# Kernel tuning notes

Measured on AMD Instinct MI355X. Metric: run time of the kernel, lower is better.

Reference implementation:

```python
import jax, jax.numpy as jnp
import numpy as np

EMBED = 256      # input_size
DOWN = 64        # expert hidden_size
NUM_EXPERTS = 10
TOPK = 2
GATE_SCALE = 0.5
LOSS_COEF = 1.0
CV_EPS = 1e-10


def setup_inputs() -> dict:
    key = jax.random.key(0)
    ks = jax.random.split(key, 6)
    B, N = 16, 4096
    x = jax.random.normal(ks[0], (B, N, EMBED), jnp.float32)
    # gating weight (Parameter in torch; random here so top-k is non-degenerate)
    w_gate = jax.random.normal(ks[1], (EMBED, NUM_EXPERTS), jnp.float32) * 0.02
    # expert MLP params: fc1 (EMBED->DOWN), relu, fc2 (DOWN->EMBED)
    w1 = jax.random.normal(ks[2], (NUM_EXPERTS, EMBED, DOWN), jnp.float32) * (1.0 / np.sqrt(EMBED))
    b1 = jnp.zeros((NUM_EXPERTS, DOWN), jnp.float32)
    w2 = jax.random.normal(ks[3], (NUM_EXPERTS, DOWN, EMBED), jnp.float32) * (1.0 / np.sqrt(DOWN))
    b2 = jnp.zeros((NUM_EXPERTS, EMBED), jnp.float32)
    return {"x": x, "w_gate": w_gate, "w1": w1, "b1": b1, "w2": w2, "b2": b2}


def _cv_squared(v):
    # torch: x.var() / (x.mean()**2 + eps), unbiased variance
    return jnp.var(v, ddof=1) / (jnp.mean(v) ** 2 + CV_EPS)


def reference(x, w_gate, w1, b1, w2, b2):
    B, N, D = x.shape
    xt = x.reshape(B * N, D)                      # (T, D)
    T = B * N

    # --- noisy top-k gating (eval mode: no noise) ---
    logits = xt @ w_gate                          # (T, E)
    top_logits, top_idx = jax.lax.top_k(logits, TOPK)
    top_gates = jax.nn.softmax(top_logits, axis=-1)
    gates = jnp.zeros((T, NUM_EXPERTS), x.dtype).at[
        jnp.arange(T)[:, None], top_idx].set(top_gates)   # (T, E), sparse rows

    importance = gates.sum(axis=0)                               # (E,)
    load = jnp.sum(gates > 0, axis=0).astype(x.dtype)            # (E,)
    aux_loss = (_cv_squared(importance) + _cv_squared(load)) * LOSS_COEF

    # --- expert FFN dispatch+combine (dense equivalent: zero gates kill terms) ---
    h = jax.nn.relu(jnp.einsum('td,edh->teh', xt, w1) + b1[None])   # (T, E, DOWN)
    ye = jnp.einsum('teh,eho->teo', h, w2) + b2[None]               # (T, E, D)
    y = jnp.einsum('te,teo->to', gates, ye)                         # (T, D)

    out = y.reshape(B, N, -1)
    # self-KD L1 loss vs zeros, computed BEFORE gate_scale is applied
    kd_loss = jnp.mean(jnp.abs(out))
    moe_loss = aux_loss + kd_loss
    return out * GATE_SCALE, moe_loss
```

## Files before the change

kernel.cpp:

```cpp
#include <hip/hip_runtime.h>
#include <hip/hip_bf16.h>

#define T_TOKENS 65536
#define EMBED 256
#define DOWN 64
#define NE 10
#define NPAIR 100
#define MAXQ 1280
#define XROW 72

typedef __attribute__((ext_vector_type(8))) short short8;
typedef __attribute__((ext_vector_type(4))) float f32x4;

__device__ inline unsigned short f2bf(float f) {
    unsigned u = __builtin_bit_cast(unsigned, f);
    u += 0x7fff + ((u >> 16) & 1);
    return (unsigned short)(u >> 16);
}
__device__ inline float bf2f(unsigned short h) {
    unsigned u = ((unsigned)h) << 16;
    return __builtin_bit_cast(float, u);
}

__global__ __launch_bounds__(256) void pack_kernel(
    const float* __restrict__ w1, const float* __restrict__ w2,
    unsigned short* __restrict__ w1ph, unsigned short* __restrict__ w1pl,
    unsigned short* __restrict__ w2ph, unsigned short* __restrict__ w2pl)
{
    int gid = blockIdx.x * 256 + threadIdx.x;
    int lane = gid & 63;
    int fid = gid >> 6;
    int n16 = lane & 15;
    int kbase = ((lane >> 4) & 3) * 8;
    if (fid < 320) {
        int kb = fid & 7, ect = fid >> 3;
        int ct = ect & 3, e = ect >> 2;
        int n = ct * 16 + n16;
        int k0 = kb * 32 + kbase;
#pragma unroll
        for (int j = 0; j < 8; ++j) {
            float v = w1[((size_t)e * EMBED + k0 + j) * DOWN + n];
            unsigned short h = f2bf(v);
            w1ph[(size_t)fid * 512 + lane * 8 + j] = h;
            w1pl[(size_t)fid * 512 + lane * 8 + j] = f2bf(v - bf2f(h));
        }
    } else if (fid < 640) {
        int f2 = fid - 320;
        int kb = f2 & 1, ect = f2 >> 1;
        int ct = ect & 15, e = ect >> 4;
        int n = ct * 16 + n16;
        int k0 = kb * 32 + kbase;
#pragma unroll
        for (int j = 0; j < 8; ++j) {
            float v = w2[((size_t)e * DOWN + k0 + j) * EMBED + n];
            unsigned short h = f2bf(v);
            w2ph[(size_t)f2 * 512 + lane * 8 + j] = h;
            w2pl[(size_t)f2 * 512 + lane * 8 + j] = f2bf(v - bf2f(h));
        }
    }
}

__global__ __launch_bounds__(256) void gating_kernel(
    const float* __restrict__ x, const float* __restrict__ wg,
    int* __restrict__ pcount, float* __restrict__ importance,
    int* __restrict__ btok, float* __restrict__ bg0)
{
    __shared__ float Xs[2][256 * 33];
    __shared__ int lcount[NPAIR];
    __shared__ int gbase[NPAIR];
    __shared__ float limp[16];
    int tid = threadIdx.x;
    if (tid < NPAIR) lcount[tid] = 0;
    if (tid < 16) limp[tid] = 0.f;

    int tokbase = blockIdx.x * 256;
    const float4* x4 = (const float4*)x;
    int rbase = tid >> 3, c4 = tid & 7;

    float4 pre[8];
#pragma unroll
    for (int i = 0; i < 8; ++i)
        pre[i] = x4[(size_t)(tokbase + i * 32 + rbase) * 64 + c4];

    float acc[NE];
#pragma unroll
    for (int e = 0; e < NE; e++) acc[e] = 0.f;

    for (int cc = 0; cc < 8; ++cc) {
        float* buf = Xs[cc & 1];
#pragma unroll
        for (int i = 0; i < 8; ++i) {
            float* d = &buf[(i * 32 + rbase) * 33 + c4 * 4];
            d[0] = pre[i].x; d[1] = pre[i].y; d[2] = pre[i].z; d[3] = pre[i].w;
        }
        if (cc < 7) {
#pragma unroll
            for (int i = 0; i < 8; ++i)
                pre[i] = x4[(size_t)(tokbase + i * 32 + rbase) * 64 + (cc + 1) * 8 + c4];
        }
        __syncthreads();
        const float* wgc = wg + cc * 32 * NE;
#pragma unroll
        for (int c = 0; c < 32; ++c) {
            float xv = buf[tid * 33 + c];
#pragma unroll
            for (int e = 0; e < NE; ++e)
                acc[e] = fmaf(xv, wgc[c * NE + e], acc[e]);
        }
    }

    float l0 = -INFINITY, l1 = -INFINITY;
    int i0 = 0, i1 = 0;
#pragma unroll
    for (int e = 0; e < NE; e++) {
        float v = acc[e];
        if (v > l0) { l1 = l0; i1 = i0; l0 = v; i0 = e; }
        else if (v > l1) { l1 = v; i1 = e; }
    }
    float ex = __expf(l1 - l0);
    float g0 = 1.f / (1.f + ex);

    int p = i0 * NE + i1;
    int lp = atomicAdd(&lcount[p], 1);
    atomicAdd(&limp[i0], g0);
    atomicAdd(&limp[i1], 1.f - g0);
    __syncthreads();
    if (tid < NPAIR) {
        int c = lcount[tid];
        gbase[tid] = c ? atomicAdd(&pcount[tid], c) : 0;
    }
    if (tid < NE) atomicAdd(&importance[tid], limp[tid]);
    __syncthreads();
    int pos = gbase[p] + lp;
    btok[p * T_TOKENS + pos] = tokbase + tid;
    bg0[p * T_TOKENS + pos] = g0;
}

__global__ void queue_kernel(const int* __restrict__ pcount,
                             int* __restrict__ qp, int* __restrict__ qs, int* __restrict__ nq)
{
    if (threadIdx.x == 0) {
        int n = 0;
        for (int p = 0; p < NPAIR; p++) {
            int c = pcount[p];
            for (int s = 0; s < c; s += 64) { qp[n] = p; qs[n] = s; n++; }
        }
        *nq = n;
    }
}

__global__ __launch_bounds__(256, 3) void expert_kernel(
    const float* __restrict__ x,
    const unsigned short* __restrict__ w1ph, const unsigned short* __restrict__ w1pl,
    const unsigned short* __restrict__ w2ph, const unsigned short* __restrict__ w2pl,
    const float* __restrict__ b1, const float* __restrict__ b2,
    const int* __restrict__ pcount, const int* __restrict__ qp, const int* __restrict__ qs,
    const int* __restrict__ nq,
    const int* __restrict__ btok, const float* __restrict__ bg0,
    float* __restrict__ out, float* __restrict__ kdpart)
{
    int bid = blockIdx.x;
    if (bid >= *nq) return;
    int p = qp[bid], s = qs[bid];
    int e0 = p / NE, e1 = p - e0 * NE;
    int m = min(64, pcount[p] - s);

    __shared__ __align__(16) unsigned short Xh[64 * XROW], Xl[64 * XROW];
    __shared__ __align__(16) unsigned short H0h[4096], H0l[4096];
    __shared__ __align__(16) unsigned short H1h[4096], H1l[4096];
    __shared__ int toks[64];
    __shared__ float gv0s[64], gv1s[64];
    __shared__ float kdw[4];

    int tid = threadIdx.x;
    if (tid < 64) {
        int v = 0; float g = 0.f;
        if (tid < m) {
            v = btok[p * T_TOKENS + s + tid];
            g = bg0[p * T_TOKENS + s + tid];
        }
        toks[tid] = v;
        gv0s[tid] = g;
        gv1s[tid] = (tid < m) ? (1.f - g) : 0.f;
    }
    __syncthreads();

    int lane = tid & 63, wv = tid >> 6;
    int ln15 = lane & 15, quad = lane >> 4;
    int srow = tid >> 2, sc0 = (tid & 3) * 16;
    const float* xrow = x + (size_t)toks[srow] * EMBED;
    bool srow_ok = srow < m;

    f32x4 a10[4], a11[4];
#pragma unroll
    for (int rt = 0; rt < 4; ++rt) { a10[rt] = (f32x4){0,0,0,0}; a11[rt] = (f32x4){0,0,0,0}; }

    const unsigned short* w1h0 = w1ph + (((size_t)e0 * 4 + wv) * 8) * 512;
    const unsigned short* w1l0 = w1pl + (((size_t)e0 * 4 + wv) * 8) * 512;
    const unsigned short* w1h1 = w1ph + (((size_t)e1 * 4 + wv) * 8) * 512;
    const unsigned short* w1l1 = w1pl + (((size_t)e1 * 4 + wv) * 8) * 512;

    for (int cc = 0; cc < 4; ++cc) {
#pragma unroll
        for (int p4 = 0; p4 < 4; ++p4) {
            int col = sc0 + p4 * 4;
            float4 v = make_float4(0.f, 0.f, 0.f, 0.f);
            if (srow_ok) v = *(const float4*)(xrow + cc * 64 + col);
            const float* vs = (const float*)&v;
            ushort4 hv, lv;
            unsigned short* hp = (unsigned short*)&hv;
            unsigned short* lp2 = (unsigned short*)&lv;
#pragma unroll
            for (int i = 0; i < 4; ++i) {
                unsigned short h = f2bf(vs[i]);
                hp[i] = h;
                lp2[i] = f2bf(vs[i] - bf2f(h));
            }
            *(ushort4*)&Xh[srow * XROW + col] = hv;
            *(ushort4*)&Xl[srow * XROW + col] = lv;
        }
        __syncthreads();
#pragma unroll
        for (int kb = 0; kb < 2; ++kb) {
            int kbg = cc * 2 + kb;
            short8 bh0 = *(const short8*)(w1h0 + (size_t)kbg * 512 + lane * 8);
            short8 bl0 = *(const short8*)(w1l0 + (size_t)kbg * 512 + lane * 8);
            short8 bh1 = *(const short8*)(w1h1 + (size_t)kbg * 512 + lane * 8);
            short8 bl1 = *(const short8*)(w1l1 + (size_t)kbg * 512 + lane * 8);
            int aoff = kb * 32 + quad * 8;
#pragma unroll
            for (int rt = 0; rt < 4; ++rt) {
                short8 ah = *(const short8*)&Xh[(rt * 16 + ln15) * XROW + aoff];
                short8 al = *(const short8*)&Xl[(rt * 16 + ln15) * XROW + aoff];
                a10[rt] = __builtin_amdgcn_mfma_f32_16x16x32_bf16(ah, bh0, a10[rt], 0, 0, 0);
                a10[rt] = __builtin_amdgcn_mfma_f32_16x16x32_bf16(ah, bl0, a10[rt], 0, 0, 0);
                a10[rt] = __builtin_amdgcn_mfma_f32_16x16x32_bf16(al, bh0, a10[rt], 0, 0, 0);
                a11[rt] = __builtin_amdgcn_mfma_f32_16x16x32_bf16(ah, bh1, a11[rt], 0, 0, 0);
                a11[rt] = __builtin_amdgcn_mfma_f32_16x16x32_bf16(ah, bl1, a11[rt], 0, 0, 0);
                a11[rt] = __builtin_amdgcn_mfma_f32_16x16x32_bf16(al, bh1, a11[rt], 0, 0, 0);
            }
        }
        __syncthreads();
    }

    {
        float b1v0 = b1[e0 * DOWN + wv * 16 + ln15];
        float b1v1 = b1[e1 * DOWN + wv * 16 + ln15];
        int kbH = wv >> 1;
        int laneH = (((wv & 1) * 2 + (ln15 >> 3)) * 16) + quad * 4;
        int jH = ln15 & 7;
#pragma unroll
        for (int rt = 0; rt < 4; ++rt) {
#pragma unroll
            for (int r = 0; r < 4; ++r) {
                int row = rt * 16 + quad * 4 + r;
                float g0 = gv0s[row], g1 = gv1s[row];
                float h0 = fmaxf(a10[rt][r] + b1v0, 0.f) * g0;
                float h1 = fmaxf(a11[rt][r] + b1v1, 0.f) * g1;
                int idx = ((rt * 2 + kbH) * 64 + laneH + r) * 8 + jH;
                unsigned short h0h = f2bf(h0);
                unsigned short h1h = f2bf(h1);
                H0h[idx] = h0h; H0l[idx] = f2bf(h0 - bf2f(h0h));
                H1h[idx] = h1h; H1l[idx] = f2bf(h1 - bf2f(h1h));
            }
        }
    }
    __syncthreads();

    float b20[4], b21[4];
#pragma unroll
    for (int ci = 0; ci < 4; ++ci) {
        b20[ci] = b2[e0 * EMBED + (wv * 4 + ci) * 16 + ln15];
        b21[ci] = b2[e1 * EMBED + (wv * 4 + ci) * 16 + ln15];
    }
    float kdacc = 0.f;
#pragma unroll
    for (int rt = 0; rt < 4; ++rt) {
        short8 ah0[2], al0[2], ah1[2], al1[2];
#pragma unroll
        for (int kb = 0; kb < 2; ++kb) {
            int base = ((rt * 2 + kb) * 64 + lane) * 8;
            ah0[kb] = *(const short8*)&H0h[base];
            al0[kb] = *(const short8*)&H0l[base];
            ah1[kb] = *(const short8*)&H1h[base];
            al1[kb] = *(const short8*)&H1l[base];
        }
        int rowb = rt * 16 + quad * 4;
        float gr0[4], gr1[4];
#pragma unroll
        for (int r = 0; r < 4; ++r) { gr0[r] = gv0s[rowb + r]; gr1[r] = gv1s[rowb + r]; }
#pragma unroll
        for (int ci = 0; ci < 4; ++ci) {
            int ct = wv * 4 + ci;
            const unsigned short* p0h = w2ph + (((size_t)e0 * 16 + ct) * 2) * 512;
            const unsigned short* p0l = w2pl + (((size_t)e0 * 16 + ct) * 2) * 512;
            const unsigned short* p1h = w2ph + (((size_t)e1 * 16 + ct) * 2) * 512;
            const unsigned short* p1l = w2pl + (((size_t)e1 * 16 + ct) * 2) * 512;
            f32x4 acc = (f32x4){0, 0, 0, 0};
#pragma unroll
            for (int kb = 0; kb < 2; ++kb) {
                short8 bh = *(const short8*)(p0h + kb * 512 + lane * 8);
                short8 bl = *(const short8*)(p0l + kb * 512 + lane * 8);
                acc = __builtin_amdgcn_mfma_f32_16x16x32_bf16(ah0[kb], bh, acc, 0, 0, 0);
                acc = __builtin_amdgcn_mfma_f32_16x16x32_bf16(ah0[kb], bl, acc, 0, 0, 0);
                acc = __builtin_amdgcn_mfma_f32_16x16x32_bf16(al0[kb], bh, acc, 0, 0, 0);
                short8 ch = *(const short8*)(p1h + kb * 512 + lane * 8);
                short8 cl = *(const short8*)(p1l + kb * 512 + lane * 8);
                acc = __builtin_amdgcn_mfma_f32_16x16x32_bf16(ah1[kb], ch, acc, 0, 0, 0);
                acc = __builtin_amdgcn_mfma_f32_16x16x32_bf16(ah1[kb], cl, acc, 0, 0, 0);
                acc = __builtin_amdgcn_mfma_f32_16x16x32_bf16(al1[kb], ch, acc, 0, 0, 0);
            }
#pragma unroll
            for (int r = 0; r < 4; ++r) {
                int row = rowb + r;
                float val = acc[r] + gr0[r] * b20[ci] + gr1[r] * b21[ci];
                if (row < m) {
                    kdacc += fabsf(val);
                    out[(size_t)toks[row] * EMBED + ct * 16 + ln15] = 0.5f * val;
                }
            }
        }
    }
#pragma unroll
    for (int o = 32; o > 0; o >>= 1) kdacc += __shfl_down(kdacc, o, 64);
    if (lane == 0) kdw[wv] = kdacc;
    __syncthreads();
    if (tid == 0)
        atomicAdd(&kdpart[bid & 63], kdw[0] + kdw[1] + kdw[2] + kdw[3]);
}

__global__ void loss_kernel(const int* __restrict__ pcount, const float* __restrict__ importance,
                            const float* __restrict__ kdpart, float* __restrict__ loss_out)
{
    if (threadIdx.x == 0) {
        float kd = 0.f;
        for (int i = 0; i < 64; i++) kd += kdpart[i];
        kd *= (1.f / (float)((size_t)T_TOKENS * EMBED));
        float load[NE];
        for (int e = 0; e < NE; e++) load[e] = 0.f;
        for (int p = 0; p < NPAIR; p++) {
            float c = (float)pcount[p];
            load[p / NE] += c;
            load[p % NE] += c;
        }
        float mi = 0.f, ml = 0.f;
        for (int e = 0; e < NE; e++) { mi += importance[e]; ml += load[e]; }
        mi *= (1.f / NE); ml *= (1.f / NE);
        float vi = 0.f, vl = 0.f;
        for (int e = 0; e < NE; e++) {
            float di = importance[e] - mi; vi += di * di;
            float dl = load[e] - ml; vl += dl * dl;
        }
        vi *= (1.f / (NE - 1)); vl *= (1.f / (NE - 1));
        float aux = vi / (mi * mi + 1e-10f) + vl / (ml * ml + 1e-10f);
        loss_out[0] = aux + kd;
    }
}

extern "C" void kernel_launch(void* const* d_in, const int* in_sizes, int n_in,
                              void* d_out, int out_size, void* d_ws, size_t ws_size,
                              hipStream_t stream)
{
    (void)in_sizes; (void)n_in; (void)out_size; (void)ws_size;
    const float* x  = (const float*)d_in[0];
    const float* wg = (const float*)d_in[1];
    const float* w1 = (const float*)d_in[2];
    const float* b1 = (const float*)d_in[3];
    const float* w2 = (const float*)d_in[4];
    const float* b2 = (const float*)d_in[5];
    float* out = (float*)d_out;

    char* ws = (char*)d_ws;
    int*   pcount     = (int*)ws;
    float* importance = (float*)(ws + 512);
    float* kdpart     = (float*)(ws + 576);
    int*   nq         = (int*)(ws + 832);
    int*   qp         = (int*)(ws + 1024);
    int*   qs         = (int*)(ws + 1024 + MAXQ * 4);
    size_t off = 16384;
    int*   btok = (int*)(ws + off);    off += (size_t)NPAIR * T_TOKENS * 4;
    float* bg0  = (float*)(ws + off);  off += (size_t)NPAIR * T_TOKENS * 4;
    unsigned short* w1ph = (unsigned short*)(ws + off); off += 327680;
    unsigned short* w1pl = (unsigned short*)(ws + off); off += 327680;
    unsigned short* w2ph = (unsigned short*)(ws + off); off += 327680;
    unsigned short* w2pl = (unsigned short*)(ws + off); off += 327680;

    hipMemsetAsync(ws, 0, 1024, stream);

    pack_kernel<<<160, 256, 0, stream>>>(w1, w2, w1ph, w1pl, w2ph, w2pl);
    gating_kernel<<<T_TOKENS / 256, 256, 0, stream>>>(x, wg, pcount, importance, btok, bg0);
    queue_kernel<<<1, 64, 0, stream>>>(pcount, qp, qs, nq);
    expert_kernel<<<1114, 256, 0, stream>>>(
        x, w1ph, w1pl, w2ph, w2pl, b1, b2, pcount, qp, qs, nq, btok, bg0, out, kdpart);
    loss_kernel<<<1, 64, 0, stream>>>(pcount, importance, kdpart, out + (size_t)T_TOKENS * EMBED);
}
```

Measured before the change: 261.0 us.

## Drop activation low-part bf16 split, parallelize gating, queue build and loss reduction

The expert kernel now rounds activations (x and hidden h) to a single bf16 value instead of a hi+lo pair. This cuts the MFMA count per product from three to two and halves LDS use for those buffers, and occupancy is raised to 4 blocks per SM. The gating kernel splits each token's 10 expert dot products across two threads, with 128 tokens per block. The serial queue and loss kernels become parallel scan and reduction versions. The trade is accuracy: activations lose their split-bf16 correction and carry only bf16 precision, which could break tolerance or flip top-k decisions near ties.

```diff
diff --git a/kernel.cpp b/kernel.cpp
--- a/kernel.cpp
+++ b/kernel.cpp
@@ -65,7 +65,7 @@
     int* __restrict__ pcount, float* __restrict__ importance,
     int* __restrict__ btok, float* __restrict__ bg0)
 {
-    __shared__ float Xs[2][256 * 33];
+    __shared__ float Xs[2][128 * 33];
     __shared__ int lcount[NPAIR];
     __shared__ int gbase[NPAIR];
     __shared__ float limp[16];
@@ -73,57 +73,69 @@
     if (tid < NPAIR) lcount[tid] = 0;
     if (tid < 16) limp[tid] = 0.f;
 
-    int tokbase = blockIdx.x * 256;
+    int tokbase = blockIdx.x * 128;
     const float4* x4 = (const float4*)x;
     int rbase = tid >> 3, c4 = tid & 7;
 
-    float4 pre[8];
-#pragma unroll
-    for (int i = 0; i < 8; ++i)
+    float4 pre[4];
+#pragma unroll
+    for (int i = 0; i < 4; ++i)
         pre[i] = x4[(size_t)(tokbase + i * 32 + rbase) * 64 + c4];
 
-    float acc[NE];
-#pragma unroll
-    for (int e = 0; e < NE; e++) acc[e] = 0.f;
+    int tk = tid >> 1;
+    int half = tid & 1;
+    float acc[5];
+#pragma unroll
+    for (int e = 0; e < 5; e++) acc[e] = 0.f;
 
     for (int cc = 0; cc < 8; ++cc) {
         float* buf = Xs[cc & 1];
 #pragma unroll
-        for (int i = 0; i < 8; ++i) {
+        for (int i = 0; i < 4; ++i) {
             float* d = &buf[(i * 32 + rbase) * 33 + c4 * 4];
             d[0] = pre[i].x; d[1] = pre[i].y; d[2] = pre[i].z; d[3] = pre[i].w;
         }
         if (cc < 7) {
 #pragma unroll
-            for (int i = 0; i < 8; ++i)
+            for (int i = 0; i < 4; ++i)
                 pre[i] = x4[(size_t)(tokbase + i * 32 + rbase) * 64 + (cc + 1) * 8 + c4];
         }
         __syncthreads();
-        const float* wgc = wg + cc * 32 * NE;
+        const float* wgc = wg + cc * 32 * NE + half * 5;
 #pragma unroll
         for (int c = 0; c < 32; ++c) {
-            float xv = buf[tid * 33 + c];
-#pragma unroll
-            for (int e = 0; e < NE; ++e)
+            float xv = buf[tk * 33 + c];
+#pragma unroll
+            for (int e = 0; e < 5; ++e)
                 acc[e] = fmaf(xv, wgc[c * NE + e], acc[e]);
         }
     }
 
-    float l0 = -INFINITY, l1 = -INFINITY;
-    int i0 = 0, i1 = 0;
-#pragma unroll
-    for (int e = 0; e < NE; e++) {
-        float v = acc[e];
-        if (v > l0) { l1 = l0; i1 = i0; l0 = v; i0 = e; }
-        else if (v > l1) { l1 = v; i1 = e; }
-    }
-    float ex = __expf(l1 - l0);
-    float g0 = 1.f / (1.f + ex);
-
-    int p = i0 * NE + i1;
-    int lp = atomicAdd(&lcount[p], 1);
-    atomicAdd(&limp[i0], g0);
-    atomicAdd(&limp[i1], 1.f - g0);
+    float oth[5];
+#pragma unroll
+    for (int e = 0; e < 5; ++e) oth[e] = __shfl_xor(acc[e], 1, 64);
+
+    int p = 0, lp = 0;
+    float g0 = 0.f;
+    if (half == 0) {
+        float l[NE];
+#pragma unroll
+        for (int e = 0; e < 5; ++e) { l[e] = acc[e]; l[5 + e] = oth[e]; }
+        float l0 = -INFINITY, l1 = -INFINITY;
+        int i0 = 0, i1 = 0;
+#pragma unroll
+        for (int e = 0; e < NE; e++) {
+            float v = l[e];
+            if (v > l0) { l1 = l0; i1 = i0; l0 = v; i0 = e; }
+            else if (v > l1) { l1 = v; i1 = e; }
+        }
+        float ex = __expf(l1 - l0);
+        g0 = 1.f / (1.f + ex);
+        p = i0 * NE + i1;
+        lp = atomicAdd(&lcount[p], 1);
+        atomicAdd(&limp[i0], g0);
+        atomicAdd(&limp[i1], 1.f - g0);
+    }
     __syncthreads();
     if (tid < NPAIR) {
         int c = lcount[tid];
@@ -131,25 +143,36 @@
     }
     if (tid < NE) atomicAdd(&importance[tid], limp[tid]);
     __syncthreads();
-    int pos = gbase[p] + lp;
-    btok[p * T_TOKENS + pos] = tokbase + tid;
-    bg0[p * T_TOKENS + pos] = g0;
-}
-
-__global__ void queue_kernel(const int* __restrict__ pcount,
-                             int* __restrict__ qp, int* __restrict__ qs, int* __restrict__ nq)
-{
-    if (threadIdx.x == 0) {
-        int n = 0;
-        for (int p = 0; p < NPAIR; p++) {
-            int c = pcount[p];
-            for (int s = 0; s < c; s += 64) { qp[n] = p; qs[n] = s; n++; }
-        }
-        *nq = n;
-    }
-}
-
-__global__ __launch_bounds__(256, 3) void expert_kernel(
+    if (half == 0) {
+        int pos = gbase[p] + lp;
+        btok[p * T_TOKENS + pos] = tokbase + tk;
+        bg0[p * T_TOKENS + pos] = g0;
+    }
+}
+
+__global__ __launch_bounds__(128) void queue_kernel(
+    const int* __restrict__ pcount,
+    int* __restrict__ qp, int* __restrict__ qs, int* __restrict__ nq)
+{
+    __shared__ int nt[128];
+    int tid = threadIdx.x;
+    int c = (tid < NPAIR) ? pcount[tid] : 0;
+    int t = (c + 63) >> 6;
+    nt[tid] = t;
+    __syncthreads();
+    for (int o = 1; o < 128; o <<= 1) {
+        int v = nt[tid];
+        int add = (tid >= o) ? nt[tid - o] : 0;
+        __syncthreads();
+        nt[tid] = v + add;
+        __syncthreads();
+    }
+    int startq = nt[tid] - t;
+    for (int i = 0; i < t; i++) { qp[startq + i] = tid; qs[startq + i] = i * 64; }
+    if (tid == 127) *nq = nt[127];
+}
+
+__global__ __launch_bounds__(256, 4) void expert_kernel(
     const float* __restrict__ x,
     const unsigned short* __restrict__ w1ph, const unsigned short* __restrict__ w1pl,
     const unsigned short* __restrict__ w2ph, const unsigned short* __restrict__ w2pl,
@@ -165,9 +188,8 @@
     int e0 = p / NE, e1 = p - e0 * NE;
     int m = min(64, pcount[p] - s);
 
-    __shared__ __align__(16) unsigned short Xh[64 * XROW], Xl[64 * XROW];
-    __shared__ __align__(16) unsigned short H0h[4096], H0l[4096];
-    __shared__ __align__(16) unsigned short H1h[4096], H1l[4096];
+    __shared__ __align__(16) unsigned short Xh[64 * XROW];
+    __shared__ __align__(16) unsigned short H0h[4096], H1h[4096];
     __shared__ int toks[64];
     __shared__ float gv0s[64], gv1s[64];
     __shared__ float kdw[4];
@@ -207,17 +229,11 @@
             float4 v = make_float4(0.f, 0.f, 0.f, 0.f);
             if (srow_ok) v = *(const float4*)(xrow + cc * 64 + col);
             const float* vs = (const float*)&v;
-            ushort4 hv, lv;
+            ushort4 hv;
             unsigned short* hp = (unsigned short*)&hv;
-            unsigned short* lp2 = (unsigned short*)&lv;
-#pragma unroll
-            for (int i = 0; i < 4; ++i) {
-                unsigned short h = f2bf(vs[i]);
-                hp[i] = h;
-                lp2[i] = f2bf(vs[i] - bf2f(h));
-            }
+#pragma unroll
+            for (int i = 0; i < 4; ++i) hp[i] = f2bf(vs[i]);
             *(ushort4*)&Xh[srow * XROW + col] = hv;
-            *(ushort4*)&Xl[srow * XROW + col] = lv;
         }
         __syncthreads();
 #pragma unroll
@@ -231,13 +247,10 @@
 #pragma unroll
             for (int rt = 0; rt < 4; ++rt) {
                 short8 ah = *(const short8*)&Xh[(rt * 16 + ln15) * XROW + aoff];
-                short8 al = *(const short8*)&Xl[(rt * 16 + ln15) * XROW + aoff];
                 a10[rt] = __builtin_amdgcn_mfma_f32_16x16x32_bf16(ah, bh0, a10[rt], 0, 0, 0);
                 a10[rt] = __builtin_amdgcn_mfma_f32_16x16x32_bf16(ah, bl0, a10[rt], 0, 0, 0);
-                a10[rt] = __builtin_amdgcn_mfma_f32_16x16x32_bf16(al, bh0, a10[rt], 0, 0, 0);
                 a11[rt] = __builtin_amdgcn_mfma_f32_16x16x32_bf16(ah, bh1, a11[rt], 0, 0, 0);
                 a11[rt] = __builtin_amdgcn_mfma_f32_16x16x32_bf16(ah, bl1, a11[rt], 0, 0, 0);
-                a11[rt] = __builtin_amdgcn_mfma_f32_16x16x32_bf16(al, bh1, a11[rt], 0, 0, 0);
             }
         }
         __syncthreads();
@@ -254,14 +267,11 @@
 #pragma unroll
             for (int r = 0; r < 4; ++r) {
                 int row = rt * 16 + quad * 4 + r;
-                float g0 = gv0s[row], g1 = gv1s[row];
-                float h0 = fmaxf(a10[rt][r] + b1v0, 0.f) * g0;
-                float h1 = fmaxf(a11[rt][r] + b1v1, 0.f) * g1;
+                float h0 = fmaxf(a10[rt][r] + b1v0, 0.f) * gv0s[row];
+                float h1 = fmaxf(a11[rt][r] + b1v1, 0.f) * gv1s[row];
                 int idx = ((rt * 2 + kbH) * 64 + laneH + r) * 8 + jH;
-                unsigned short h0h = f2bf(h0);
-                unsigned short h1h = f2bf(h1);
-                H0h[idx] = h0h; H0l[idx] = f2bf(h0 - bf2f(h0h));
-                H1h[idx] = h1h; H1l[idx] = f2bf(h1 - bf2f(h1h));
+                H0h[idx] = f2bf(h0);
+                H1h[idx] = f2bf(h1);
             }
         }
     }
@@ -276,14 +286,12 @@
     float kdacc = 0.f;
 #pragma unroll
     for (int rt = 0; rt < 4; ++rt) {
-        short8 ah0[2], al0[2], ah1[2], al1[2];
+        short8 ah0[2], ah1[2];
 #pragma unroll
         for (int kb = 0; kb < 2; ++kb) {
             int base = ((rt * 2 + kb) * 64 + lane) * 8;
             ah0[kb] = *(const short8*)&H0h[base];
-            al0[kb] = *(const short8*)&H0l[base];
             ah1[kb] = *(const short8*)&H1h[base];
-            al1[kb] = *(const short8*)&H1l[base];
         }
         int rowb = rt * 16 + quad * 4;
         float gr0[4], gr1[4];
@@ -303,12 +311,10 @@
                 short8 bl = *(const short8*)(p0l + kb * 512 + lane * 8);
                 acc = __builtin_amdgcn_mfma_f32_16x16x32_bf16(ah0[kb], bh, acc, 0, 0, 0);
                 acc = __builtin_amdgcn_mfma_f32_16x16x32_bf16(ah0[kb], bl, acc, 0, 0, 0);
-                acc = __builtin_amdgcn_mfma_f32_16x16x32_bf16(al0[kb], bh, acc, 0, 0, 0);
                 short8 ch = *(const short8*)(p1h + kb * 512 + lane * 8);
                 short8 cl = *(const short8*)(p1l + kb * 512 + lane * 8);
                 acc = __builtin_amdgcn_mfma_f32_16x16x32_bf16(ah1[kb], ch, acc, 0, 0, 0);
                 acc = __builtin_amdgcn_mfma_f32_16x16x32_bf16(ah1[kb], cl, acc, 0, 0, 0);
-                acc = __builtin_amdgcn_mfma_f32_16x16x32_bf16(al1[kb], ch, acc, 0, 0, 0);
             }
 #pragma unroll
             for (int r = 0; r < 4; ++r) {
@@ -329,27 +335,32 @@
         atomicAdd(&kdpart[bid & 63], kdw[0] + kdw[1] + kdw[2] + kdw[3]);
 }
 
-__global__ void loss_kernel(const int* __restrict__ pcount, const float* __restrict__ importance,
-                            const float* __restrict__ kdpart, float* __restrict__ loss_out)
-{
-    if (threadIdx.x == 0) {
-        float kd = 0.f;
-        for (int i = 0; i < 64; i++) kd += kdpart[i];
+__global__ __launch_bounds__(64) void loss_kernel(
+    const int* __restrict__ pcount, const float* __restrict__ importance,
+    const float* __restrict__ kdpart, float* __restrict__ loss_out)
+{
+    __shared__ float simp[16], sload[16];
+    int tid = threadIdx.x;
+    float kd = kdpart[tid];
+#pragma unroll
+    for (int o = 32; o > 0; o >>= 1) kd += __shfl_down(kd, o, 64);
+    if (tid < NE) {
+        float l = 0.f;
+        for (int j = 0; j < NE; j++)
+            l += (float)(pcount[tid * NE + j] + pcount[j * NE + tid]);
+        sload[tid] = l;
+        simp[tid] = importance[tid];
+    }
+    __syncthreads();
+    if (tid == 0) {
         kd *= (1.f / (float)((size_t)T_TOKENS * EMBED));
-        float load[NE];
-        for (int e = 0; e < NE; e++) load[e] = 0.f;
-        for (int p = 0; p < NPAIR; p++) {
-            float c = (float)pcount[p];
-            load[p / NE] += c;
-            load[p % NE] += c;
-        }
         float mi = 0.f, ml = 0.f;
-        for (int e = 0; e < NE; e++) { mi += importance[e]; ml += load[e]; }
+        for (int e = 0; e < NE; e++) { mi += simp[e]; ml += sload[e]; }
         mi *= (1.f / NE); ml *= (1.f / NE);
         float vi = 0.f, vl = 0.f;
         for (int e = 0; e < NE; e++) {
-            float di = importance[e] - mi; vi += di * di;
-            float dl = load[e] - ml; vl += dl * dl;
+            float di = simp[e] - mi; vi += di * di;
+            float dl = sload[e] - ml; vl += dl * dl;
         }
         vi *= (1.f / (NE - 1)); vl *= (1.f / (NE - 1));
         float aux = vi / (mi * mi + 1e-10f) + vl / (ml * ml + 1e-10f);
@@ -388,8 +399,8 @@
     hipMemsetAsync(ws, 0, 1024, stream);
 
     pack_kernel<<<160, 256, 0, stream>>>(w1, w2, w1ph, w1pl, w2ph, w2pl);
-    gating_kernel<<<T_TOKENS / 256, 256, 0, stream>>>(x, wg, pcount, importance, btok, bg0);
-    queue_kernel<<<1, 64, 0, stream>>>(pcount, qp, qs, nq);
+    gating_kernel<<<T_TOKENS / 128, 256, 0, stream>>>(x, wg, pcount, importance, btok, bg0);
+    queue_kernel<<<1, 128, 0, stream>>>(pcount, qp, qs, nq);
     expert_kernel<<<1114, 256, 0, stream>>>(
         x, w1ph, w1pl, w2ph, w2pl, b1, b2, pcount, qp, qs, nq, btok, bg0, out, kdpart);
     loss_kernel<<<1, 64, 0, stream>>>(pcount, importance, kdpart, out + (size_t)T_TOKENS * EMBED);
```

New measurement: 268.3 us. 1.03x slower.
